# Kernel tuning notes

Hardware: AMD Instinct MI355X
Metric: run time of the kernel (lower is better)

The kernel has to match this reference:

```python
import jax, jax.numpy as jnp
import numpy as np

LEAKY_ALPHA = 0.2  # tf.nn.leaky_relu default

B, S, E = 16, 4096, 768
H, A = 4, 128  # segments_amount (heads), attention_dimension


def setup_inputs() -> dict:
    key = jax.random.key(0)
    k0, k1, k2 = jax.random.split(key, 3)
    x = jax.random.normal(k0, (B, S, E), dtype=jnp.float32)
    # Per-head MLP params, Glorot-ish scaling
    W1 = jax.random.normal(k1, (H, E, A), dtype=jnp.float32) * (1.0 / np.sqrt(E))
    b1 = jnp.zeros((H, A), dtype=jnp.float32)
    W2 = jax.random.normal(k2, (H, A, E), dtype=jnp.float32) * (1.0 / np.sqrt(A))
    b2 = jnp.zeros((H, E), dtype=jnp.float32)
    return {"x": x, "W1": W1, "b1": b1, "W2": W2, "b2": b2}


def reference(x, W1, b1, W2, b2):
    # Batched over heads h: Dense->LeakyReLU->Dense
    h = jnp.einsum('bse,hea->bhsa', x, W1) + b1[None, :, None, :]
    h = jnp.where(h >= 0, h, LEAKY_ALPHA * h)
    logits = jnp.einsum('bhsa,hae->bhse', h, W2) + b2[None, :, None, :]
    # Softmax over sequence axis (axis=1 in original per-head [B,S,E])
    weights = jax.nn.softmax(logits, axis=2)  # [B,H,S,E]
    # Attention-weighted sum over sequence -> [B,H,E]
    segment_embeddings = jnp.einsum('bse,bhse->bhe', x, weights)
    return segment_embeddings
```

## Files before the change

### kernel.cpp

```cpp
#include <hip/hip_runtime.h>
#include <hip/hip_bf16.h>

#define B_ 16
#define S_ 4096
#define E_ 768
#define H_ 4
#define A_ 128

constexpr float ALPHA = 0.2f;
constexpr float LOG2E = 1.44269504088896340736f;

typedef __attribute__((ext_vector_type(4))) float f32x4;
typedef __attribute__((ext_vector_type(8))) short bf16x8;

__device__ __forceinline__ unsigned short f2bf(float f) {
    union { float f; unsigned int u; } v;
    v.f = f;
    unsigned int u = v.u;
    unsigned int r = (u + 0x7FFFu + ((u >> 16) & 1u)) >> 16;
    return (unsigned short)r;
}

__global__ __launch_bounds__(256) void k_prep1(const float* __restrict__ w1,
                                               unsigned short* __restrict__ w1t) {
    __shared__ unsigned short t[64 * 65];
    int bid = blockIdx.x;
    int ta = bid & 1;
    int te = (bid >> 1) % 12;
    int h  = bid / 24;
    const float* src = w1 + (size_t)h * E_ * A_;
    unsigned short* dst = w1t + (size_t)h * A_ * E_;
    int tid = threadIdx.x;
#pragma unroll
    for (int it = 0; it < 16; ++it) {
        int idx = it * 256 + tid;
        int r = idx >> 6, c = idx & 63;
        t[r * 65 + c] = f2bf(src[(size_t)(te * 64 + r) * A_ + ta * 64 + c]);
    }
    __syncthreads();
#pragma unroll
    for (int it = 0; it < 16; ++it) {
        int idx = it * 256 + tid;
        int a = idx >> 6, e = idx & 63;
        dst[(size_t)(ta * 64 + a) * E_ + te * 64 + e] = t[e * 65 + a];
    }
}

__global__ __launch_bounds__(256) void k_prep2(const float* __restrict__ w2,
                                               unsigned short* __restrict__ w2t) {
    __shared__ unsigned short t[64 * 65];
    int bid = blockIdx.x;
    int te = bid % 12;
    int ta = (bid / 12) & 1;
    int h  = bid / 24;
    const float* src = w2 + (size_t)h * A_ * E_;
    unsigned short* dst = w2t + (size_t)h * E_ * A_;
    int tid = threadIdx.x;
#pragma unroll
    for (int it = 0; it < 16; ++it) {
        int idx = it * 256 + tid;
        int r = idx >> 6, c = idx & 63;
        t[r * 65 + c] = f2bf(src[(size_t)(ta * 64 + r) * E_ + te * 64 + c] * LOG2E);
    }
    __syncthreads();
#pragma unroll
    for (int it = 0; it < 16; ++it) {
        int idx = it * 256 + tid;
        int e = idx >> 6, a = idx & 63;
        dst[(size_t)(te * 64 + e) * A_ + ta * 64 + a] = t[a * 65 + e];
    }
}

__global__ __launch_bounds__(256) void k_fused(
    const float* __restrict__ x, const unsigned short* __restrict__ w1t,
    const float* __restrict__ b1, const unsigned short* __restrict__ w2t,
    float* __restrict__ part_z, float* __restrict__ part_o) {

    int bid = blockIdx.x;
    int wid = (bid & 7) * 256 + (bid >> 3);
    const int h  = wid & 3;
    const int st = (wid >> 2) & 31;
    const int b  = wid >> 7;
    const int s0 = st * 128;

    const int tid = threadIdx.x;
    const int wave = tid >> 6, lane = tid & 63;
    const int lr = lane & 15, lg = lane >> 4;

    __shared__ unsigned short smem[16384];
    unsigned short* stg_a = smem;
    unsigned short* stg_b = smem + 8192;

    f32x4 acc[2][8];
#pragma unroll
    for (int i = 0; i < 2; ++i)
#pragma unroll
        for (int j = 0; j < 8; ++j) acc[i][j] = (f32x4)0.0f;

    const float* xb = x + ((size_t)b * S_ + s0) * E_;
    const unsigned short* w1h = w1t + (size_t)h * A_ * E_;

#pragma unroll 1
    for (int e0 = 0; e0 < E_; e0 += 64) {
        __syncthreads();
#pragma unroll
        for (int it = 0; it < 4; ++it) {
            int ci = tid + it * 256;
            int r = ci >> 3, c = ci & 7;
            int byte = (r * 128 + c * 16) ^ ((r & 7) << 4);
            const float* ap = xb + (size_t)r * E_ + e0 + c * 8;
            f32x4 v0 = *(const f32x4*)ap;
            f32x4 v1 = *(const f32x4*)(ap + 4);
            bf16x8 av;
#pragma unroll
            for (int j = 0; j < 4; ++j) {
                av[j]     = (short)f2bf(v0[j]);
                av[4 + j] = (short)f2bf(v1[j]);
            }
            *(bf16x8*)((char*)stg_a + byte) = av;
            *(bf16x8*)((char*)stg_b + byte) = *(const bf16x8*)(w1h + (size_t)r * E_ + e0 + c * 8);
        }
        __syncthreads();
#pragma unroll
        for (int kk = 0; kk < 2; ++kk) {
            bf16x8 afr[2], bfr[8];
#pragma unroll
            for (int sf = 0; sf < 2; ++sf) {
                int row = wave * 32 + sf * 16 + lr;
                afr[sf] = *(const bf16x8*)((char*)stg_a + ((row * 128 + kk * 64 + lg * 16) ^ ((row & 7) << 4)));
            }
#pragma unroll
            for (int nf = 0; nf < 8; ++nf) {
                int row = nf * 16 + lr;
                bfr[nf] = *(const bf16x8*)((char*)stg_b + ((row * 128 + kk * 64 + lg * 16) ^ ((row & 7) << 4)));
            }
#pragma unroll
            for (int nf = 0; nf < 8; ++nf) {
                acc[0][nf] = __builtin_amdgcn_mfma_f32_16x16x32_bf16(afr[0], bfr[nf], acc[0][nf], 0, 0, 0);
                acc[1][nf] = __builtin_amdgcn_mfma_f32_16x16x32_bf16(afr[1], bfr[nf], acc[1][nf], 0, 0, 0);
            }
        }
    }

    __syncthreads();
    unsigned short* hmt = smem;
#pragma unroll
    for (int nf = 0; nf < 8; ++nf) {
        float bias = b1[h * A_ + nf * 16 + lr];
#pragma unroll
        for (int sf = 0; sf < 2; ++sf) {
#pragma unroll
            for (int j = 0; j < 4; ++j) {
                float v = acc[sf][nf][j] + bias;
                v = v >= 0.0f ? v : ALPHA * v;
                int srow = wave * 32 + sf * 16 + lg * 4 + j;
                int a = nf * 16 + lr;
                int byte = (srow * 256 + a * 2) ^ ((srow & 7) << 4);
                *(unsigned short*)((char*)hmt + byte) = f2bf(v);
            }
        }
    }
    __syncthreads();

    const int ebase_w = wave * 32;
#pragma unroll 1
    for (int p = 0; p < 3; ++p) {
        bf16x8 w2f[2][2][4];
#pragma unroll
        for (int e2 = 0; e2 < 2; ++e2)
#pragma unroll
            for (int nf = 0; nf < 2; ++nf) {
                int e = (2 * p + e2) * 128 + ebase_w + nf * 16 + lr;
                const unsigned short* wp = w2t + ((size_t)h * E_ + e) * A_ + lg * 8;
#pragma unroll
                for (int ks = 0; ks < 4; ++ks)
                    w2f[e2][nf][ks] = *(const bf16x8*)(wp + ks * 32);
            }
        f32x4 zz[4], oo[4];
#pragma unroll
        for (int q = 0; q < 4; ++q) { zz[q] = (f32x4)0.0f; oo[q] = (f32x4)0.0f; }

#pragma unroll 2
        for (int itr = 0; itr < 8; ++itr) {
            bf16x8 hfr[4];
#pragma unroll
            for (int ks = 0; ks < 4; ++ks) {
                int srow = itr * 16 + lr;
                hfr[ks] = *(const bf16x8*)((char*)hmt + ((srow * 256 + ks * 64 + lg * 16) ^ ((srow & 7) << 4)));
            }
            f32x4 lac[4];
#pragma unroll
            for (int q = 0; q < 4; ++q) lac[q] = (f32x4)0.0f;
#pragma unroll
            for (int ks = 0; ks < 4; ++ks)
#pragma unroll
                for (int e2 = 0; e2 < 2; ++e2)
#pragma unroll
                    for (int nf = 0; nf < 2; ++nf)
                        lac[e2 * 2 + nf] = __builtin_amdgcn_mfma_f32_16x16x32_bf16(
                            w2f[e2][nf][ks], hfr[ks], lac[e2 * 2 + nf], 0, 0, 0);
#pragma unroll
            for (int e2 = 0; e2 < 2; ++e2)
#pragma unroll
                for (int nf = 0; nf < 2; ++nf) {
                    int q = e2 * 2 + nf;
                    const float* xp = xb + (size_t)(itr * 16 + lr) * E_
                                    + (2 * p + e2) * 128 + ebase_w + nf * 16 + lg * 4;
                    f32x4 xv = *(const f32x4*)xp;
                    f32x4 pv;
#pragma unroll
                    for (int j = 0; j < 4; ++j) pv[j] = exp2f(lac[q][j]);
                    zz[q] += pv;
                    oo[q] += pv * xv;
                }
        }
#pragma unroll
        for (int q = 0; q < 4; ++q)
#pragma unroll
            for (int j = 0; j < 4; ++j) {
#pragma unroll
                for (int msk = 1; msk < 16; msk <<= 1) {
                    zz[q][j] += __shfl_xor(zz[q][j], msk);
                    oo[q][j] += __shfl_xor(oo[q][j], msk);
                }
            }
        if (lr == 0) {
#pragma unroll
            for (int e2 = 0; e2 < 2; ++e2)
#pragma unroll
                for (int nf = 0; nf < 2; ++nf) {
                    int q = e2 * 2 + nf;
                    int e = (2 * p + e2) * 128 + ebase_w + nf * 16 + lg * 4;
                    size_t base = ((size_t)(b * H_ + h) * E_ + e) * 32 + st;
#pragma unroll
                    for (int j = 0; j < 4; ++j) {
                        part_z[base + (size_t)j * 32] = zz[q][j];
                        part_o[base + (size_t)j * 32] = oo[q][j];
                    }
                }
        }
    }
}

__global__ __launch_bounds__(256) void k_merge(const float* __restrict__ part_z,
                                               const float* __restrict__ part_o,
                                               float* __restrict__ out) {
    int idx = blockIdx.x * 256 + threadIdx.x;
    if (idx >= B_ * H_ * E_) return;
    const float* pz = part_z + (size_t)idx * 32;
    const float* po = part_o + (size_t)idx * 32;
    float z = 0.f, o = 0.f;
#pragma unroll
    for (int q = 0; q < 8; ++q) {
        f32x4 a = *(const f32x4*)(pz + q * 4);
        f32x4 c = *(const f32x4*)(po + q * 4);
        z += (a[0] + a[1]) + (a[2] + a[3]);
        o += (c[0] + c[1]) + (c[2] + c[3]);
    }
    out[idx] = o / z;
}

extern "C" void kernel_launch(void* const* d_in, const int* in_sizes, int n_in,
                              void* d_out, int out_size, void* d_ws, size_t ws_size,
                              hipStream_t stream) {
    const float* x  = (const float*)d_in[0];
    const float* w1 = (const float*)d_in[1];
    const float* b1 = (const float*)d_in[2];
    const float* w2 = (const float*)d_in[3];
    float* out = (float*)d_out;

    char* ws = (char*)d_ws;
    float*          part_z = (float*)ws;
    float*          part_o = (float*)(ws + 6291456);
    unsigned short* w1t    = (unsigned short*)(ws + 12582912);
    unsigned short* w2t    = (unsigned short*)(ws + 13369344);

    k_prep1<<<dim3(96),   256, 0, stream>>>(w1, w1t);
    k_prep2<<<dim3(96),   256, 0, stream>>>(w2, w2t);
    k_fused<<<dim3(2048), 256, 0, stream>>>(x, w1t, b1, w2t, part_z, part_o);
    k_merge<<<dim3(192),  256, 0, stream>>>(part_z, part_o, out);
}
```

Baseline: 609.8 us.

## Split fused MLP kernel into two stages with global bf16 hidden buffer

```diff
diff --git a/kernel.cpp b/kernel.cpp
--- a/kernel.cpp
+++ b/kernel.cpp
@@ -19,6 +19,13 @@
     unsigned int u = v.u;
     unsigned int r = (u + 0x7FFFu + ((u >> 16) & 1u)) >> 16;
     return (unsigned short)r;
+}
+
+__device__ __forceinline__ unsigned int pk2bf(float lo, float hi) {
+    __hip_bfloat162 h2 = __float22bfloat162_rn(make_float2(lo, hi));
+    union { __hip_bfloat162 h; unsigned int u; } c;
+    c.h = h2;
+    return c.u;
 }
 
 __global__ __launch_bounds__(256) void k_prep1(const float* __restrict__ w1,
@@ -71,10 +78,9 @@
     }
 }
 
-__global__ __launch_bounds__(256) void k_fused(
+__global__ __launch_bounds__(512, 4) void k_stage1(
     const float* __restrict__ x, const unsigned short* __restrict__ w1t,
-    const float* __restrict__ b1, const unsigned short* __restrict__ w2t,
-    float* __restrict__ part_z, float* __restrict__ part_o) {
+    const float* __restrict__ b1, unsigned short* __restrict__ hm) {
 
     int bid = blockIdx.x;
     int wid = (bid & 7) * 256 + (bid >> 3);
@@ -84,161 +90,187 @@
     const int s0 = st * 128;
 
     const int tid = threadIdx.x;
-    const int wave = tid >> 6, lane = tid & 63;
+    const int wv = tid >> 6, lane = tid & 63;
     const int lr = lane & 15, lg = lane >> 4;
-
-    __shared__ unsigned short smem[16384];
-    unsigned short* stg_a = smem;
-    unsigned short* stg_b = smem + 8192;
-
-    f32x4 acc[2][8];
-#pragma unroll
-    for (int i = 0; i < 2; ++i)
-#pragma unroll
-        for (int j = 0; j < 8; ++j) acc[i][j] = (f32x4)0.0f;
+    const int sw = wv & 1, aw = wv >> 1;
+
+    __shared__ unsigned short bufA[128 * 64];
+    __shared__ unsigned short bufB[128 * 64];
+
+    const int ar = tid >> 2;
+    const int ac = tid & 3;
+    const float* xp = x + ((size_t)b * S_ + s0 + ar) * E_ + ac * 16;
+    const unsigned short* wp = w1t + ((size_t)h * A_ + ar) * E_ + ac * 8;
+
+    f32x4 acc[4][2];
+#pragma unroll
+    for (int i = 0; i < 4; ++i)
+#pragma unroll
+        for (int j = 0; j < 2; ++j) acc[i][j] = (f32x4)0.0f;
+
+    f32x4 xreg[4];
+    bf16x8 wreg[2];
+#pragma unroll
+    for (int l = 0; l < 4; ++l) xreg[l] = *(const f32x4*)(xp + l * 4);
+#pragma unroll
+    for (int l = 0; l < 2; ++l) wreg[l] = *(const bf16x8*)(wp + l * 32);
+
+#pragma unroll 1
+    for (int ks = 0; ks < 12; ++ks) {
+        if (ks) __syncthreads();
+#pragma unroll
+        for (int l = 0; l < 4; ++l) {
+            uint2 p;
+            p.x = pk2bf(xreg[l][0], xreg[l][1]);
+            p.y = pk2bf(xreg[l][2], xreg[l][3]);
+            int byte = (ar * 128 + (ac * 4 + l) * 8) ^ ((ar & 7) << 4);
+            *(uint2*)((char*)bufA + byte) = p;
+        }
+#pragma unroll
+        for (int l = 0; l < 2; ++l) {
+            int byte = (ar * 128 + (ac + l * 4) * 16) ^ ((ar & 7) << 4);
+            *(bf16x8*)((char*)bufB + byte) = wreg[l];
+        }
+        __syncthreads();
+        if (ks < 11) {
+            const float* xq = xp + (ks + 1) * 64;
+#pragma unroll
+            for (int l = 0; l < 4; ++l) xreg[l] = *(const f32x4*)(xq + l * 4);
+            const unsigned short* wq = wp + (ks + 1) * 64;
+#pragma unroll
+            for (int l = 0; l < 2; ++l) wreg[l] = *(const bf16x8*)(wq + l * 32);
+        }
+#pragma unroll
+        for (int kk = 0; kk < 2; ++kk) {
+            bf16x8 xf[4], wf[2];
+#pragma unroll
+            for (int sf = 0; sf < 4; ++sf) {
+                int r = sw * 64 + sf * 16 + lr;
+                xf[sf] = *(const bf16x8*)((char*)bufA + ((r * 128 + kk * 64 + lg * 16) ^ ((r & 7) << 4)));
+            }
+#pragma unroll
+            for (int nf = 0; nf < 2; ++nf) {
+                int r = aw * 32 + nf * 16 + lr;
+                wf[nf] = *(const bf16x8*)((char*)bufB + ((r * 128 + kk * 64 + lg * 16) ^ ((r & 7) << 4)));
+            }
+#pragma unroll
+            for (int sf = 0; sf < 4; ++sf)
+#pragma unroll
+                for (int nf = 0; nf < 2; ++nf)
+                    acc[sf][nf] = __builtin_amdgcn_mfma_f32_16x16x32_bf16(
+                        wf[nf], xf[sf], acc[sf][nf], 0, 0, 0);
+        }
+    }
+
+    const size_t hb = ((size_t)(b * H_ + h) * S_ + s0 + sw * 64) * A_ + aw * 32;
+#pragma unroll
+    for (int nf = 0; nf < 2; ++nf) {
+        f32x4 bv = *(const f32x4*)(b1 + h * A_ + aw * 32 + nf * 16 + lg * 4);
+#pragma unroll
+        for (int sf = 0; sf < 4; ++sf) {
+            f32x4 v = acc[sf][nf] + bv;
+#pragma unroll
+            for (int j = 0; j < 4; ++j) v[j] = v[j] >= 0.0f ? v[j] : ALPHA * v[j];
+            uint2 p;
+            p.x = pk2bf(v[0], v[1]);
+            p.y = pk2bf(v[2], v[3]);
+            *(uint2*)(hm + hb + (size_t)(sf * 16 + lr) * A_ + nf * 16 + lg * 4) = p;
+        }
+    }
+}
+
+__global__ __launch_bounds__(256, 4) void k_stage2(
+    const float* __restrict__ x, const unsigned short* __restrict__ hm,
+    const unsigned short* __restrict__ w2t,
+    float* __restrict__ part_z, float* __restrict__ part_o) {
+
+    int bid = blockIdx.x;
+    int wid = (bid & 7) * 256 + (bid >> 3);
+    const int h  = wid & 3;
+    const int sc = (wid >> 2) & 31;
+    const int b  = wid >> 7;
+    const int s0 = sc * 128;
+
+    const int tid = threadIdx.x;
+    const int wv = tid >> 6, lane = tid & 63;
+    const int lr = lane & 15, lg = lane >> 4;
+
+    __shared__ unsigned short hmt[128 * 128];
+
+    {
+        const unsigned short* hp = hm + ((size_t)(b * H_ + h) * S_ + s0) * A_;
+        int r = tid >> 1;
+        int c = tid & 1;
+#pragma unroll
+        for (int l = 0; l < 8; ++l) {
+            int ch = c * 8 + l;
+            bf16x8 v = *(const bf16x8*)(hp + (size_t)r * A_ + ch * 8);
+            int byte = (r * 256 + ch * 16) ^ ((r & 7) << 4);
+            *(bf16x8*)((char*)hmt + byte) = v;
+        }
+    }
+    __syncthreads();
 
     const float* xb = x + ((size_t)b * S_ + s0) * E_;
-    const unsigned short* w1h = w1t + (size_t)h * A_ * E_;
+    const unsigned short* w2h = w2t + (size_t)h * E_ * A_;
+    const size_t pbase = (size_t)(b * H_ + h) * E_ * 32 + sc;
 
 #pragma unroll 1
-    for (int e0 = 0; e0 < E_; e0 += 64) {
-        __syncthreads();
-#pragma unroll
-        for (int it = 0; it < 4; ++it) {
-            int ci = tid + it * 256;
-            int r = ci >> 3, c = ci & 7;
-            int byte = (r * 128 + c * 16) ^ ((r & 7) << 4);
-            const float* ap = xb + (size_t)r * E_ + e0 + c * 8;
-            f32x4 v0 = *(const f32x4*)ap;
-            f32x4 v1 = *(const f32x4*)(ap + 4);
-            bf16x8 av;
-#pragma unroll
-            for (int j = 0; j < 4; ++j) {
-                av[j]     = (short)f2bf(v0[j]);
-                av[4 + j] = (short)f2bf(v1[j]);
-            }
-            *(bf16x8*)((char*)stg_a + byte) = av;
-            *(bf16x8*)((char*)stg_b + byte) = *(const bf16x8*)(w1h + (size_t)r * E_ + e0 + c * 8);
-        }
-        __syncthreads();
-#pragma unroll
-        for (int kk = 0; kk < 2; ++kk) {
-            bf16x8 afr[2], bfr[8];
-#pragma unroll
-            for (int sf = 0; sf < 2; ++sf) {
-                int row = wave * 32 + sf * 16 + lr;
-                afr[sf] = *(const bf16x8*)((char*)stg_a + ((row * 128 + kk * 64 + lg * 16) ^ ((row & 7) << 4)));
-            }
-#pragma unroll
-            for (int nf = 0; nf < 8; ++nf) {
-                int row = nf * 16 + lr;
-                bfr[nf] = *(const bf16x8*)((char*)stg_b + ((row * 128 + kk * 64 + lg * 16) ^ ((row & 7) << 4)));
-            }
-#pragma unroll
-            for (int nf = 0; nf < 8; ++nf) {
-                acc[0][nf] = __builtin_amdgcn_mfma_f32_16x16x32_bf16(afr[0], bfr[nf], acc[0][nf], 0, 0, 0);
-                acc[1][nf] = __builtin_amdgcn_mfma_f32_16x16x32_bf16(afr[1], bfr[nf], acc[1][nf], 0, 0, 0);
-            }
-        }
-    }
-
-    __syncthreads();
-    unsigned short* hmt = smem;
-#pragma unroll
-    for (int nf = 0; nf < 8; ++nf) {
-        float bias = b1[h * A_ + nf * 16 + lr];
-#pragma unroll
-        for (int sf = 0; sf < 2; ++sf) {
-#pragma unroll
-            for (int j = 0; j < 4; ++j) {
-                float v = acc[sf][nf][j] + bias;
-                v = v >= 0.0f ? v : ALPHA * v;
-                int srow = wave * 32 + sf * 16 + lg * 4 + j;
-                int a = nf * 16 + lr;
-                int byte = (srow * 256 + a * 2) ^ ((srow & 7) << 4);
-                *(unsigned short*)((char*)hmt + byte) = f2bf(v);
-            }
-        }
-    }
-    __syncthreads();
-
-    const int ebase_w = wave * 32;
-#pragma unroll 1
-    for (int p = 0; p < 3; ++p) {
-        bf16x8 w2f[2][2][4];
-#pragma unroll
-        for (int e2 = 0; e2 < 2; ++e2)
-#pragma unroll
-            for (int nf = 0; nf < 2; ++nf) {
-                int e = (2 * p + e2) * 128 + ebase_w + nf * 16 + lr;
-                const unsigned short* wp = w2t + ((size_t)h * E_ + e) * A_ + lg * 8;
-#pragma unroll
-                for (int ks = 0; ks < 4; ++ks)
-                    w2f[e2][nf][ks] = *(const bf16x8*)(wp + ks * 32);
-            }
-        f32x4 zz[4], oo[4];
-#pragma unroll
-        for (int q = 0; q < 4; ++q) { zz[q] = (f32x4)0.0f; oo[q] = (f32x4)0.0f; }
+    for (int et = 0; et < 6; ++et) {
+        const int e0 = et * 128 + wv * 32;
+        bf16x8 w2f[2][4];
+#pragma unroll
+        for (int nf = 0; nf < 2; ++nf) {
+            const unsigned short* q = w2h + (size_t)(e0 + nf * 16 + lr) * A_ + lg * 8;
+#pragma unroll
+            for (int k4 = 0; k4 < 4; ++k4) w2f[nf][k4] = *(const bf16x8*)(q + k4 * 32);
+        }
+        f32x4 zz[2], oo[2];
+#pragma unroll
+        for (int nf = 0; nf < 2; ++nf) { zz[nf] = (f32x4)0.0f; oo[nf] = (f32x4)0.0f; }
 
 #pragma unroll 2
         for (int itr = 0; itr < 8; ++itr) {
-            bf16x8 hfr[4];
-#pragma unroll
-            for (int ks = 0; ks < 4; ++ks) {
-                int srow = itr * 16 + lr;
-                hfr[ks] = *(const bf16x8*)((char*)hmt + ((srow * 256 + ks * 64 + lg * 16) ^ ((srow & 7) << 4)));
-            }
-            f32x4 lac[4];
-#pragma unroll
-            for (int q = 0; q < 4; ++q) lac[q] = (f32x4)0.0f;
-#pragma unroll
-            for (int ks = 0; ks < 4; ++ks)
-#pragma unroll
-                for (int e2 = 0; e2 < 2; ++e2)
-#pragma unroll
-                    for (int nf = 0; nf < 2; ++nf)
-                        lac[e2 * 2 + nf] = __builtin_amdgcn_mfma_f32_16x16x32_bf16(
-                            w2f[e2][nf][ks], hfr[ks], lac[e2 * 2 + nf], 0, 0, 0);
-#pragma unroll
-            for (int e2 = 0; e2 < 2; ++e2)
-#pragma unroll
-                for (int nf = 0; nf < 2; ++nf) {
-                    int q = e2 * 2 + nf;
-                    const float* xp = xb + (size_t)(itr * 16 + lr) * E_
-                                    + (2 * p + e2) * 128 + ebase_w + nf * 16 + lg * 4;
-                    f32x4 xv = *(const f32x4*)xp;
-                    f32x4 pv;
-#pragma unroll
-                    for (int j = 0; j < 4; ++j) pv[j] = exp2f(lac[q][j]);
-                    zz[q] += pv;
-                    oo[q] += pv * xv;
+            int srow = itr * 16 + lr;
+            bf16x8 hf[4];
+#pragma unroll
+            for (int k4 = 0; k4 < 4; ++k4)
+                hf[k4] = *(const bf16x8*)((char*)hmt +
+                          ((srow * 256 + (k4 * 32 + lg * 8) * 2) ^ ((srow & 7) << 4)));
+            f32x4 lac[2];
+            lac[0] = (f32x4)0.0f; lac[1] = (f32x4)0.0f;
+#pragma unroll
+            for (int k4 = 0; k4 < 4; ++k4) {
+                lac[0] = __builtin_amdgcn_mfma_f32_16x16x32_bf16(w2f[0][k4], hf[k4], lac[0], 0, 0, 0);
+                lac[1] = __builtin_amdgcn_mfma_f32_16x16x32_bf16(w2f[1][k4], hf[k4], lac[1], 0, 0, 0);
+            }
+#pragma unroll
+            for (int nf = 0; nf < 2; ++nf) {
+                const float* xq = xb + (size_t)srow * E_ + e0 + nf * 16 + lg * 4;
+                f32x4 xv = *(const f32x4*)xq;
+                f32x4 pv;
+#pragma unroll
+                for (int j = 0; j < 4; ++j) pv[j] = exp2f(lac[nf][j]);
+                zz[nf] += pv;
+                oo[nf] += pv * xv;
+            }
+        }
+#pragma unroll
+        for (int nf = 0; nf < 2; ++nf)
+#pragma unroll
+            for (int j = 0; j < 4; ++j) {
+                float zv = zz[nf][j], ov = oo[nf][j];
+#pragma unroll
+                for (int msk = 1; msk < 16; msk <<= 1) {
+                    zv += __shfl_xor(zv, msk);
+                    ov += __shfl_xor(ov, msk);
                 }
-        }
-#pragma unroll
-        for (int q = 0; q < 4; ++q)
-#pragma unroll
-            for (int j = 0; j < 4; ++j) {
-#pragma unroll
-                for (int msk = 1; msk < 16; msk <<= 1) {
-                    zz[q][j] += __shfl_xor(zz[q][j], msk);
-                    oo[q][j] += __shfl_xor(oo[q][j], msk);
+                if (lr == 0) {
+                    int e = e0 + nf * 16 + lg * 4 + j;
+                    part_z[pbase + (size_t)e * 32] = zv;
+                    part_o[pbase + (size_t)e * 32] = ov;
                 }
             }
-        if (lr == 0) {
-#pragma unroll
-            for (int e2 = 0; e2 < 2; ++e2)
-#pragma unroll
-                for (int nf = 0; nf < 2; ++nf) {
-                    int q = e2 * 2 + nf;
-                    int e = (2 * p + e2) * 128 + ebase_w + nf * 16 + lg * 4;
-                    size_t base = ((size_t)(b * H_ + h) * E_ + e) * 32 + st;
-#pragma unroll
-                    for (int j = 0; j < 4; ++j) {
-                        part_z[base + (size_t)j * 32] = zz[q][j];
-                        part_o[base + (size_t)j * 32] = oo[q][j];
-                    }
-                }
-        }
     }
 }
 
@@ -270,13 +302,15 @@
     float* out = (float*)d_out;
 
     char* ws = (char*)d_ws;
-    float*          part_z = (float*)ws;
-    float*          part_o = (float*)(ws + 6291456);
-    unsigned short* w1t    = (unsigned short*)(ws + 12582912);
-    unsigned short* w2t    = (unsigned short*)(ws + 13369344);
-
-    k_prep1<<<dim3(96),   256, 0, stream>>>(w1, w1t);
-    k_prep2<<<dim3(96),   256, 0, stream>>>(w2, w2t);
-    k_fused<<<dim3(2048), 256, 0, stream>>>(x, w1t, b1, w2t, part_z, part_o);
-    k_merge<<<dim3(192),  256, 0, stream>>>(part_z, part_o, out);
-}
+    unsigned short* hmw    = (unsigned short*)ws;
+    unsigned short* w1t    = (unsigned short*)(ws + 67108864);
+    unsigned short* w2t    = (unsigned short*)(ws + 67895296);
+    float*          part_z = (float*)(ws + 68681728);
+    float*          part_o = (float*)(ws + 74973184);
+
+    k_prep1 <<<dim3(96),   256, 0, stream>>>(w1, w1t);
+    k_prep2 <<<dim3(96),   256, 0, stream>>>(w2, w2t);
+    k_stage1<<<dim3(2048), 512, 0, stream>>>(x, w1t, b1, hmw);
+    k_stage2<<<dim3(2048), 256, 0, stream>>>(x, hmw, w2t, part_z, part_o);
+    k_merge <<<dim3(192),  256, 0, stream>>>(part_z, part_o, out);
+}
```

Measured after the change: 547.1 us. -10.3%, faster.
